# Kernel optimization log

Hardware: AMD Instinct MI355X
Metric: run time of the kernel (lower is better)

## Reference

```python
import jax, jax.numpy as jnp
import numpy as np

B, C, H, W, OC, K = 8, 256, 120, 120, 256, 3


def setup_inputs() -> dict:
    key = jax.random.key(0)
    ks = jax.random.split(key, 6)
    x = jax.random.normal(ks[0], (B, C, H, W), jnp.float32)
    y = jax.random.normal(ks[1], (B, C, H, W), jnp.float32)
    # generate_kernel: 1x1 conv in_yC -> in_xC (weight stored as (out, in))
    gen_w = jax.random.normal(ks[2], (C, C), jnp.float32) * (1.0 / np.sqrt(C))
    gen_b = jax.random.normal(ks[3], (C,), jnp.float32) * 0.01
    # fuse: 3x3 conv in_xC -> out_C, padding 1
    fuse_w = jax.random.normal(ks[4], (OC, C, 3, 3), jnp.float32) * (1.0 / np.sqrt(C * 9))
    fuse_b = jax.random.normal(ks[5], (OC,), jnp.float32) * 0.01
    return {"x": x, "y": y, "gen_w": gen_w, "gen_b": gen_b,
            "fuse_w": fuse_w, "fuse_b": fuse_b}


def reference(x, y, gen_w, gen_b, fuse_w, fuse_b):
    b, c, h, w = x.shape
    # AdaptiveAvgPool2d(K): H,W divisible by K -> uniform average pooling
    yp = y.reshape(b, c, K, h // K, K, w // K).mean(axis=(3, 5))  # (B,C,K,K)
    # 1x1 conv to generate per-sample per-channel kernels
    kernel = jnp.einsum('oc,bcij->boij', gen_w, yp) + gen_b[None, :, None, None]
    # dynamic depthwise conv: groups = B*C, padding 1 (cross-correlation, as torch)
    xg = x.reshape(1, b * c, h, w)
    kg = kernel.reshape(b * c, 1, K, K)
    dn = jax.lax.conv_dimension_numbers(xg.shape, kg.shape, ('NCHW', 'OIHW', 'NCHW'))
    out = jax.lax.conv_general_dilated(
        xg, kg, window_strides=(1, 1), padding=((1, 1), (1, 1)),
        dimension_numbers=dn, feature_group_count=b * c)
    out = out.reshape(b, c, h, w)
    # fuse: dense 3x3 conv C -> OC, padding 1, with bias
    dn2 = jax.lax.conv_dimension_numbers(out.shape, fuse_w.shape, ('NCHW', 'OIHW', 'NCHW'))
    res = jax.lax.conv_general_dilated(
        out, fuse_w, window_strides=(1, 1), padding=((1, 1), (1, 1)),
        dimension_numbers=dn2)
    return res + fuse_b[None, :, None, None]
```

## Files before the change

### kernel.cpp

```cpp
#include <hip/hip_runtime.h>
#include <hip/hip_bf16.h>
#include <stdint.h>

#define TB 8
#define TC 256
#define TH 120
#define TW 120
#define THW 14400
#define TOC 256
#define PH 122
#define PW 122

typedef short bf16x8 __attribute__((ext_vector_type(8)));
typedef float f32x4 __attribute__((ext_vector_type(4)));

#define OUTP_BYTES ((size_t)TB * PH * PW * TC * 2)
#define YP_OFF     OUTP_BYTES
#define DK_OFF     (YP_OFF + (size_t)TB * TC * 9 * 4)
#define WP_OFF     (DK_OFF + (size_t)TB * TC * 9 * 4)

__global__ void zero_halo_kernel(char* __restrict__ outP) {
    int i = blockIdx.x * 256 + threadIdx.x;
    int pos_idx = i >> 5, part = i & 31;
    int b = pos_idx / 484; int k = pos_idx - b * 484;
    int h, w;
    if (k < 122)      { h = 0;   w = k; }
    else if (k < 244) { h = 121; w = k - 122; }
    else { int m = k - 244; h = 1 + (m >> 1); w = (m & 1) ? 121 : 0; }
    size_t pos = ((size_t)b * PH + h) * PW + w;
    uint4 z; z.x = 0u; z.y = 0u; z.z = 0u; z.w = 0u;
    *(uint4*)(outP + pos * 512 + part * 16) = z;
}

__global__ __launch_bounds__(128) void pool_kernel(const float* __restrict__ y,
                                                   float* __restrict__ yp) {
    int bc = blockIdx.x, t = threadIdx.x;
    __shared__ float pr[120][4];
    __shared__ float p2[9][8];
    const float* src = y + (size_t)bc * THW;
    if (t < 120) {
        const float4* row = (const float4*)(src + t * TW);
        float s0 = 0.f, s1 = 0.f, s2 = 0.f;
        #pragma unroll
        for (int j = 0; j < 10; ++j)  { float4 v = row[j]; s0 += (v.x + v.y) + (v.z + v.w); }
        #pragma unroll
        for (int j = 10; j < 20; ++j) { float4 v = row[j]; s1 += (v.x + v.y) + (v.z + v.w); }
        #pragma unroll
        for (int j = 20; j < 30; ++j) { float4 v = row[j]; s2 += (v.x + v.y) + (v.z + v.w); }
        pr[t][0] = s0; pr[t][1] = s1; pr[t][2] = s2;
    }
    __syncthreads();
    if (t < 72) {
        int bin = t >> 3, ch = t & 7;
        int bh = bin / 3, bw = bin - bh * 3;
        float a = 0.f;
        #pragma unroll
        for (int r = 0; r < 5; ++r) a += pr[bh * 40 + ch * 5 + r][bw];
        p2[bin][ch] = a;
    }
    __syncthreads();
    if (t < 9) {
        float a = 0.f;
        #pragma unroll
        for (int j = 0; j < 8; ++j) a += p2[t][j];
        yp[bc * 9 + t] = a * (1.f / 1600.f);
    }
}

__global__ __launch_bounds__(256) void gen_kernel(const float* __restrict__ yp,
        const float* __restrict__ gen_w, const float* __restrict__ gen_b,
        float* __restrict__ dk) {
    int blk = blockIdx.x;
    int b = blk >> 3, ocg = blk & 7;
    int t = threadIdx.x;
    int ocl = t & 31, cseg = t >> 5;
    int oc = ocg * 32 + ocl;
    __shared__ float yps[TC * 9];
    for (int i = t; i < TC * 9; i += 256) yps[i] = yp[b * TC * 9 + i];
    __syncthreads();
    float acc[9];
    #pragma unroll
    for (int j = 0; j < 9; ++j) acc[j] = 0.f;
    const float* wrow = gen_w + (size_t)oc * TC + cseg * 32;
    for (int c = 0; c < 32; ++c) {
        float w = wrow[c];
        const float* yrow = &yps[(cseg * 32 + c) * 9];
        #pragma unroll
        for (int j = 0; j < 9; ++j) acc[j] += w * yrow[j];
    }
    __shared__ float red[8][32][9];
    #pragma unroll
    for (int j = 0; j < 9; ++j) red[cseg][ocl][j] = acc[j];
    __syncthreads();
    for (int st = 4; st > 0; st >>= 1) {
        if (cseg < st) {
            #pragma unroll
            for (int j = 0; j < 9; ++j) red[cseg][ocl][j] += red[cseg + st][ocl][j];
        }
        __syncthreads();
    }
    if (cseg == 0) {
        float bias = gen_b[oc];
        #pragma unroll
        for (int j = 0; j < 9; ++j)
            dk[((size_t)b * TC + oc) * 9 + j] = red[0][ocl][j] + bias;
    }
}

__global__ __launch_bounds__(1024) void dw_kernel(const float* __restrict__ x,
        const float* __restrict__ dk, __hip_bfloat16* __restrict__ outP) {
    int bid = blockIdx.x;
    int hs = bid & 7;
    int cc = (bid >> 3) & 7;
    int b  = bid >> 6;
    int t = threadIdx.x;
    int c  = t >> 5;
    int wq = t & 31;
    bool active = wq < 30;
    int w0 = wq * 4;
    int cg = cc * 32 + c;
    const float* xp = x + (size_t)(b * TC + cg) * THW;
    const float* dkp = dk + (size_t)(b * TC + cg) * 9;
    float k0[3], k1[3], k2[3];
    #pragma unroll
    for (int j = 0; j < 3; ++j) { k0[j] = dkp[j]; k1[j] = dkp[3 + j]; k2[j] = dkp[6 + j]; }

    __shared__ __align__(16) __hip_bfloat16 stage[2][2][32][124];

    int h0 = hs * 15;
    float A[6], B[6], C[6];
    auto loadrow = [&](int hh, float* V) {
        if (hh < 0 || hh >= TH) {
            #pragma unroll
            for (int j = 0; j < 6; ++j) V[j] = 0.f;
            return;
        }
        const float* row = xp + hh * TW;
        float4 v = *(const float4*)(row + w0);
        V[1] = v.x; V[2] = v.y; V[3] = v.z; V[4] = v.w;
        V[0] = (wq > 0)  ? row[w0 - 1] : 0.f;
        V[5] = (wq < 29) ? row[w0 + 4] : 0.f;
    };
    auto comp = [&](int r, int par, int sub) {
        if (!active) return;
        loadrow(h0 + r + 1, C);
        ushort4 pk;
        #pragma unroll
        for (int i = 0; i < 4; ++i) {
            float o = A[i] * k0[0] + A[i + 1] * k0[1] + A[i + 2] * k0[2]
                    + B[i] * k1[0] + B[i + 1] * k1[1] + B[i + 2] * k1[2]
                    + C[i] * k2[0] + C[i + 1] * k2[1] + C[i + 2] * k2[2];
            __hip_bfloat16 hb = __float2bfloat16(o);
            ushort u = *(ushort*)&hb;
            if (i == 0) pk.x = u; else if (i == 1) pk.y = u;
            else if (i == 2) pk.z = u; else pk.w = u;
        }
        *(ushort4*)&stage[par][sub][c][w0] = pk;
        #pragma unroll
        for (int j = 0; j < 6; ++j) { A[j] = B[j]; B[j] = C[j]; }
    };
    auto flushrow = [&](int r, int par, int sub, int tt) {
        int w = tt >> 2, part = tt & 3;
        ushort vals[8];
        #pragma unroll
        for (int j = 0; j < 8; ++j) vals[j] = *(const ushort*)&stage[par][sub][part * 8 + j][w];
        uint4 o;
        o.x = (uint)vals[0] | ((uint)vals[1] << 16);
        o.y = (uint)vals[2] | ((uint)vals[3] << 16);
        o.z = (uint)vals[4] | ((uint)vals[5] << 16);
        o.w = (uint)vals[6] | ((uint)vals[7] << 16);
        size_t pos = ((size_t)b * PH + (h0 + r + 1)) * PW + (w + 1);
        *(uint4*)((char*)outP + pos * 512 + cc * 64 + part * 16) = o;
    };

    if (active) { loadrow(h0 - 1, A); loadrow(h0, B); }
    comp(0, 0, 0); comp(1, 0, 1);
    __syncthreads();
    #pragma unroll 1
    for (int p = 1; p < 8; ++p) {
        int r0 = 2 * p;
        comp(r0, p & 1, 0);
        if (r0 + 1 < 15) comp(r0 + 1, p & 1, 1);
        if (t < 960) {
            int fr = t >= 480 ? 1 : 0;
            int tt = t - fr * 480;
            flushrow(2 * (p - 1) + fr, (p - 1) & 1, fr, tt);
        }
        __syncthreads();
    }
    if (t < 480) flushrow(14, 1, 0, t);
}

__global__ void wprep_kernel(const float* __restrict__ fuse_w, __hip_bfloat16* __restrict__ Wp) {
    int i = blockIdx.x * 256 + threadIdx.x;
    int ij = i >> 16;
    int oc = (i >> 8) & 255;
    int c  = i & 255;
    Wp[i] = __float2bfloat16(fuse_w[(oc * 256 + c) * 9 + ij]);
}

typedef const __attribute__((address_space(1))) char* gas_t;
typedef __attribute__((address_space(3))) char* las_t;
__device__ __forceinline__ void gload16(const char* g, char* l) {
    __builtin_amdgcn_global_load_lds((gas_t)g, (las_t)l, 16, 0, 0);
}

__global__ __launch_bounds__(256, 2) void gemm_kernel(
        const __hip_bfloat16* __restrict__ outP,
        const __hip_bfloat16* __restrict__ Wp,
        const float* __restrict__ fuse_b,
        float* __restrict__ res) {
    __shared__ __align__(16) char lds[2][32768];
    const int t = threadIdx.x;
    const int lane = t & 63;
    const int wv = t >> 6;
    const int wo = wv >> 1;
    const int wm = wv & 1;

    const int bid0 = blockIdx.x;
    const int logical = (bid0 & 7) * 225 + (bid0 >> 3);
    const int bn = logical & 1;
    const int bm = logical >> 1;

    const char* gI = (const char*)outP;
    const char* gW = (const char*)Wp;

    const int rbp = (((lane & 7) ^ (lane >> 3)) << 4);
    int srcI[4], srcW[4];
    #pragma unroll
    for (int q = 0; q < 4; ++q) {
        int p = (q * 4 + wv) * 8 + (lane >> 3);
        int m = bm * 128 + p;
        int b = m / THW; int r = m - b * THW;
        int h = r / TW;  int w = r - h * TW;
        srcI[q] = (((b * PH + h) * PW + w) << 9) + rbp;
        srcW[q] = ((bn * 128 + p) << 9) + rbp;
    }
    const int segBase = wv * 1024;

    int aWb[4], aWs[4], aIb[4], aIs[4];
    #pragma unroll
    for (int i = 0; i < 4; ++i) {
        int rw = wo * 64 + i * 16 + (lane & 15);
        aWb[i] = rw * 128; aWs[i] = (rw & 7) << 4;
        int ri = wm * 64 + i * 16 + (lane & 15);
        aIb[i] = ri * 128; aIs[i] = (ri & 7) << 4;
    }
    const int klo = (lane >> 4) << 4;

    f32x4 acc[4][4];
    #pragma unroll
    for (int i = 0; i < 4; ++i) {
        #pragma unroll
        for (int j = 0; j < 4; ++j) {
            f32x4 z = {0.f, 0.f, 0.f, 0.f};
            acc[i][j] = z;
        }
    }

    auto step_offs = [&](int s, int& offI, int& offW) {
        int ij = s >> 2;
        int c0b = (s & 3) << 7;
        int di = ij / 3, dj = ij - (ij / 3) * 3;
        offI = ((di * PW + dj) << 9) + c0b;
        offW = (ij << 17) + c0b;
    };
    auto STAGE = [&](int buf, int s) {
        int offI, offW; step_offs(s, offI, offW);
        char* LI = &lds[buf][0];
        char* LW = &lds[buf][16384];
        #pragma unroll
        for (int q = 0; q < 4; ++q) {
            gload16(gI + srcI[q] + offI, LI + segBase + q * 4096);
            gload16(gW + srcW[q] + offW, LW + segBase + q * 4096);
        }
    };
    auto COMPUTE = [&](int buf) {
        const char* LI = &lds[buf][0];
        const char* LW = &lds[buf][16384];
        #pragma unroll
        for (int kk = 0; kk < 2; ++kk) {
            int ck = kk * 64 + klo;
            bf16x8 wf[4], iff[4];
            #pragma unroll
            for (int i = 0; i < 4; ++i)
                wf[i] = *(const bf16x8*)(LW + aWb[i] + (ck ^ aWs[i]));
            #pragma unroll
            for (int i = 0; i < 4; ++i)
                iff[i] = *(const bf16x8*)(LI + aIb[i] + (ck ^ aIs[i]));
            __builtin_amdgcn_s_setprio(1);
            #pragma unroll
            for (int o = 0; o < 4; ++o) {
                #pragma unroll
                for (int mi = 0; mi < 4; ++mi)
                    acc[o][mi] = __builtin_amdgcn_mfma_f32_16x16x32_bf16(
                        wf[o], iff[mi], acc[o][mi], 0, 0, 0);
            }
            __builtin_amdgcn_s_setprio(0);
        }
    };

    STAGE(0, 0);
    #pragma unroll 1
    for (int s = 0; s < 35; ++s) {
        int cur = s & 1;
        STAGE(cur ^ 1, s + 1);
        asm volatile("s_waitcnt vmcnt(8)" ::: "memory");
        __builtin_amdgcn_s_barrier();
        asm volatile("" ::: "memory");
        COMPUTE(cur);
        asm volatile("" ::: "memory");
        __builtin_amdgcn_s_barrier();
        asm volatile("" ::: "memory");
    }
    asm volatile("s_waitcnt vmcnt(0)" ::: "memory");
    __builtin_amdgcn_s_barrier();
    asm volatile("" ::: "memory");
    COMPUTE(1);

    int baseM[4];
    #pragma unroll
    for (int mt = 0; mt < 4; ++mt) {
        int m = bm * 128 + wm * 64 + mt * 16 + (lane & 15);
        int b = m / THW; int r = m - b * THW;
        baseM[mt] = b * (TOC * THW) + r;
    }
    const int ocb0 = bn * 128 + wo * 64 + ((lane >> 4) << 2);
    float bias[4][4];
    #pragma unroll
    for (int o = 0; o < 4; ++o) {
        #pragma unroll
        for (int g = 0; g < 4; ++g)
            bias[o][g] = fuse_b[ocb0 + o * 16 + g];
    }
    #pragma unroll
    for (int o = 0; o < 4; ++o) {
        #pragma unroll
        for (int mt = 0; mt < 4; ++mt) {
            #pragma unroll
            for (int g = 0; g < 4; ++g)
                res[baseM[mt] + (ocb0 + o * 16 + g) * THW] = acc[o][mt][g] + bias[o][g];
        }
    }
}

extern "C" void kernel_launch(void* const* d_in, const int* in_sizes, int n_in,
                              void* d_out, int out_size, void* d_ws, size_t ws_size,
                              hipStream_t stream) {
    const float* x      = (const float*)d_in[0];
    const float* y      = (const float*)d_in[1];
    const float* gen_w  = (const float*)d_in[2];
    const float* gen_b  = (const float*)d_in[3];
    const float* fuse_w = (const float*)d_in[4];
    const float* fuse_b = (const float*)d_in[5];
    float* out = (float*)d_out;
    char* ws = (char*)d_ws;

    __hip_bfloat16* outP = (__hip_bfloat16*)(ws);
    float* yp = (float*)(ws + YP_OFF);
    float* dk = (float*)(ws + DK_OFF);
    __hip_bfloat16* Wp = (__hip_bfloat16*)(ws + WP_OFF);

    zero_halo_kernel<<<484, 256, 0, stream>>>((char*)outP);
    pool_kernel<<<TB * TC, 128, 0, stream>>>(y, yp);
    gen_kernel<<<64, 256, 0, stream>>>(yp, gen_w, gen_b, dk);
    wprep_kernel<<<2304, 256, 0, stream>>>(fuse_w, Wp);
    dw_kernel<<<512, 1024, 0, stream>>>(x, dk, outP);
    gemm_kernel<<<1800, 256, 0, stream>>>(outP, Wp, fuse_b, out);
}
```

Before: 223.9 us.

## Merge halo-zero and weight-prep kernels; restructure GEMM to 2 waves single-buffered

Fuses the halo zeroing and weight conversion into one launch, saving a kernel launch. The implicit-GEMM kernel drops from 4 waves with double-buffered LDS to 2 waves per block. Each wave now computes a larger 128x64 tile with 32 accumulators, and the block uses a single 32KB LDS buffer with no overlap between loads and MFMA. The intent is more register-level reuse and more resident blocks per CU, at the cost of serializing global-to-LDS loads against compute.

```diff
diff --git a/kernel.cpp b/kernel.cpp
--- a/kernel.cpp
+++ b/kernel.cpp
@@ -19,17 +19,28 @@
 #define DK_OFF     (YP_OFF + (size_t)TB * TC * 9 * 4)
 #define WP_OFF     (DK_OFF + (size_t)TB * TC * 9 * 4)
 
-__global__ void zero_halo_kernel(char* __restrict__ outP) {
-    int i = blockIdx.x * 256 + threadIdx.x;
-    int pos_idx = i >> 5, part = i & 31;
-    int b = pos_idx / 484; int k = pos_idx - b * 484;
-    int h, w;
-    if (k < 122)      { h = 0;   w = k; }
-    else if (k < 244) { h = 121; w = k - 122; }
-    else { int m = k - 244; h = 1 + (m >> 1); w = (m & 1) ? 121 : 0; }
-    size_t pos = ((size_t)b * PH + h) * PW + w;
-    uint4 z; z.x = 0u; z.y = 0u; z.z = 0u; z.w = 0u;
-    *(uint4*)(outP + pos * 512 + part * 16) = z;
+__global__ void prep_kernel(const float* __restrict__ fuse_w,
+                            __hip_bfloat16* __restrict__ Wp,
+                            char* __restrict__ outP) {
+    int blk = blockIdx.x;
+    if (blk < 484) {
+        int i = blk * 256 + threadIdx.x;
+        int pos_idx = i >> 5, part = i & 31;
+        int b = pos_idx / 484; int k = pos_idx - b * 484;
+        int h, w;
+        if (k < 122)      { h = 0;   w = k; }
+        else if (k < 244) { h = 121; w = k - 122; }
+        else { int m = k - 244; h = 1 + (m >> 1); w = (m & 1) ? 121 : 0; }
+        size_t pos = ((size_t)b * PH + h) * PW + w;
+        uint4 z; z.x = 0u; z.y = 0u; z.z = 0u; z.w = 0u;
+        *(uint4*)(outP + pos * 512 + part * 16) = z;
+    } else {
+        int i = (blk - 484) * 256 + threadIdx.x;
+        int ij = i >> 16;
+        int oc = (i >> 8) & 255;
+        int c  = i & 255;
+        Wp[i] = __float2bfloat16(fuse_w[(oc * 256 + c) * 9 + ij]);
+    }
 }
 
 __global__ __launch_bounds__(128) void pool_kernel(const float* __restrict__ y,
@@ -191,31 +202,26 @@
     if (t < 480) flushrow(14, 1, 0, t);
 }
 
-__global__ void wprep_kernel(const float* __restrict__ fuse_w, __hip_bfloat16* __restrict__ Wp) {
-    int i = blockIdx.x * 256 + threadIdx.x;
-    int ij = i >> 16;
-    int oc = (i >> 8) & 255;
-    int c  = i & 255;
-    Wp[i] = __float2bfloat16(fuse_w[(oc * 256 + c) * 9 + ij]);
-}
-
 typedef const __attribute__((address_space(1))) char* gas_t;
 typedef __attribute__((address_space(3))) char* las_t;
 __device__ __forceinline__ void gload16(const char* g, char* l) {
     __builtin_amdgcn_global_load_lds((gas_t)g, (las_t)l, 16, 0, 0);
 }
-
-__global__ __launch_bounds__(256, 2) void gemm_kernel(
+__device__ __forceinline__ void barrier_() {
+    asm volatile("" ::: "memory");
+    __builtin_amdgcn_s_barrier();
+    asm volatile("" ::: "memory");
+}
+
+__global__ __launch_bounds__(128) void gemm_kernel(
         const __hip_bfloat16* __restrict__ outP,
         const __hip_bfloat16* __restrict__ Wp,
         const float* __restrict__ fuse_b,
         float* __restrict__ res) {
-    __shared__ __align__(16) char lds[2][32768];
+    __shared__ __align__(16) char lds[32768];
     const int t = threadIdx.x;
     const int lane = t & 63;
-    const int wv = t >> 6;
-    const int wo = wv >> 1;
-    const int wm = wv & 1;
+    const int wn = t >> 6;
 
     const int bid0 = blockIdx.x;
     const int logical = (bid0 & 7) * 225 + (bid0 >> 3);
@@ -225,121 +231,101 @@
     const char* gI = (const char*)outP;
     const char* gW = (const char*)Wp;
 
-    const int rbp = (((lane & 7) ^ (lane >> 3)) << 4);
-    int srcI[4], srcW[4];
-    #pragma unroll
-    for (int q = 0; q < 4; ++q) {
-        int p = (q * 4 + wv) * 8 + (lane >> 3);
+    const int srb = (((t & 7) ^ ((t >> 3) & 7)) << 4);
+    int srcA[8], srcB[8];
+    #pragma unroll
+    for (int q = 0; q < 8; ++q) {
+        int p = q * 16 + (t >> 3);
         int m = bm * 128 + p;
         int b = m / THW; int r = m - b * THW;
         int h = r / TW;  int w = r - h * TW;
-        srcI[q] = (((b * PH + h) * PW + w) << 9) + rbp;
-        srcW[q] = ((bn * 128 + p) << 9) + rbp;
-    }
-    const int segBase = wv * 1024;
-
-    int aWb[4], aWs[4], aIb[4], aIs[4];
-    #pragma unroll
-    for (int i = 0; i < 4; ++i) {
-        int rw = wo * 64 + i * 16 + (lane & 15);
-        aWb[i] = rw * 128; aWs[i] = (rw & 7) << 4;
-        int ri = wm * 64 + i * 16 + (lane & 15);
-        aIb[i] = ri * 128; aIs[i] = (ri & 7) << 4;
-    }
+        srcA[q] = (((b * PH + h) * PW + w) << 9) + srb;
+        srcB[q] = ((bn * 128 + p) << 9) + srb;
+    }
+
+    const int sw  = (lane & 7) << 4;
     const int klo = (lane >> 4) << 4;
-
-    f32x4 acc[4][4];
-    #pragma unroll
-    for (int i = 0; i < 4; ++i) {
-        #pragma unroll
-        for (int j = 0; j < 4; ++j) {
-            f32x4 z = {0.f, 0.f, 0.f, 0.f};
-            acc[i][j] = z;
-        }
-    }
-
-    auto step_offs = [&](int s, int& offI, int& offW) {
+    int aA[8], aB[4];
+    #pragma unroll
+    for (int f = 0; f < 8; ++f) aA[f] = (f * 16 + (lane & 15)) * 128;
+    #pragma unroll
+    for (int g = 0; g < 4; ++g) aB[g] = 16384 + (wn * 64 + g * 16 + (lane & 15)) * 128;
+
+    f32x4 acc[8][4];
+    #pragma unroll
+    for (int f = 0; f < 8; ++f) {
+        #pragma unroll
+        for (int g = 0; g < 4; ++g) { f32x4 z = {0.f,0.f,0.f,0.f}; acc[f][g] = z; }
+    }
+
+    auto STAGE = [&](int s) {
         int ij = s >> 2;
         int c0b = (s & 3) << 7;
-        int di = ij / 3, dj = ij - (ij / 3) * 3;
-        offI = ((di * PW + dj) << 9) + c0b;
-        offW = (ij << 17) + c0b;
-    };
-    auto STAGE = [&](int buf, int s) {
-        int offI, offW; step_offs(s, offI, offW);
-        char* LI = &lds[buf][0];
-        char* LW = &lds[buf][16384];
-        #pragma unroll
-        for (int q = 0; q < 4; ++q) {
-            gload16(gI + srcI[q] + offI, LI + segBase + q * 4096);
-            gload16(gW + srcW[q] + offW, LW + segBase + q * 4096);
-        }
-    };
-    auto COMPUTE = [&](int buf) {
-        const char* LI = &lds[buf][0];
-        const char* LW = &lds[buf][16384];
+        int di = ij / 3, dj = ij - di * 3;
+        int offI = ((di * PW + dj) << 9) + c0b;
+        int offW = (ij << 17) + c0b;
+        #pragma unroll
+        for (int q = 0; q < 8; ++q)
+            gload16(gI + srcA[q] + offI, lds + q * 2048 + t * 16);
+        #pragma unroll
+        for (int q = 0; q < 8; ++q)
+            gload16(gW + srcB[q] + offW, lds + 16384 + q * 2048 + t * 16);
+    };
+    auto COMPUTE = [&]() {
         #pragma unroll
         for (int kk = 0; kk < 2; ++kk) {
-            int ck = kk * 64 + klo;
-            bf16x8 wf[4], iff[4];
-            #pragma unroll
-            for (int i = 0; i < 4; ++i)
-                wf[i] = *(const bf16x8*)(LW + aWb[i] + (ck ^ aWs[i]));
-            #pragma unroll
-            for (int i = 0; i < 4; ++i)
-                iff[i] = *(const bf16x8*)(LI + aIb[i] + (ck ^ aIs[i]));
+            int cx = (kk * 64 + klo) ^ sw;
+            bf16x8 fA[8], fB[4];
+            #pragma unroll
+            for (int f = 0; f < 8; ++f) fA[f] = *(const bf16x8*)(lds + aA[f] + cx);
+            #pragma unroll
+            for (int g = 0; g < 4; ++g) fB[g] = *(const bf16x8*)(lds + aB[g] + cx);
             __builtin_amdgcn_s_setprio(1);
             #pragma unroll
-            for (int o = 0; o < 4; ++o) {
+            for (int f = 0; f < 8; ++f) {
                 #pragma unroll
-                for (int mi = 0; mi < 4; ++mi)
-                    acc[o][mi] = __builtin_amdgcn_mfma_f32_16x16x32_bf16(
-                        wf[o], iff[mi], acc[o][mi], 0, 0, 0);
+                for (int g = 0; g < 4; ++g)
+                    acc[f][g] = __builtin_amdgcn_mfma_f32_16x16x32_bf16(
+                        fB[g], fA[f], acc[f][g], 0, 0, 0);
             }
             __builtin_amdgcn_s_setprio(0);
         }
     };
 
-    STAGE(0, 0);
+    STAGE(0);
     #pragma unroll 1
     for (int s = 0; s < 35; ++s) {
-        int cur = s & 1;
-        STAGE(cur ^ 1, s + 1);
-        asm volatile("s_waitcnt vmcnt(8)" ::: "memory");
-        __builtin_amdgcn_s_barrier();
-        asm volatile("" ::: "memory");
-        COMPUTE(cur);
-        asm volatile("" ::: "memory");
-        __builtin_amdgcn_s_barrier();
-        asm volatile("" ::: "memory");
+        asm volatile("s_waitcnt vmcnt(0)" ::: "memory");
+        barrier_();
+        COMPUTE();
+        barrier_();
+        STAGE(s + 1);
     }
     asm volatile("s_waitcnt vmcnt(0)" ::: "memory");
-    __builtin_amdgcn_s_barrier();
-    asm volatile("" ::: "memory");
-    COMPUTE(1);
-
-    int baseM[4];
-    #pragma unroll
-    for (int mt = 0; mt < 4; ++mt) {
-        int m = bm * 128 + wm * 64 + mt * 16 + (lane & 15);
+    barrier_();
+    COMPUTE();
+
+    int baseM[8];
+    #pragma unroll
+    for (int f = 0; f < 8; ++f) {
+        int m = bm * 128 + f * 16 + (lane & 15);
         int b = m / THW; int r = m - b * THW;
-        baseM[mt] = b * (TOC * THW) + r;
-    }
-    const int ocb0 = bn * 128 + wo * 64 + ((lane >> 4) << 2);
+        baseM[f] = b * (TOC * THW) + r;
+    }
+    const int oc0 = bn * 128 + wn * 64 + ((lane >> 4) << 2);
     float bias[4][4];
     #pragma unroll
-    for (int o = 0; o < 4; ++o) {
-        #pragma unroll
-        for (int g = 0; g < 4; ++g)
-            bias[o][g] = fuse_b[ocb0 + o * 16 + g];
-    }
-    #pragma unroll
-    for (int o = 0; o < 4; ++o) {
-        #pragma unroll
-        for (int mt = 0; mt < 4; ++mt) {
-            #pragma unroll
-            for (int g = 0; g < 4; ++g)
-                res[baseM[mt] + (ocb0 + o * 16 + g) * THW] = acc[o][mt][g] + bias[o][g];
+    for (int g = 0; g < 4; ++g) {
+        #pragma unroll
+        for (int j = 0; j < 4; ++j) bias[g][j] = fuse_b[oc0 + g * 16 + j];
+    }
+    #pragma unroll
+    for (int g = 0; g < 4; ++g) {
+        #pragma unroll
+        for (int f = 0; f < 8; ++f) {
+            #pragma unroll
+            for (int j = 0; j < 4; ++j)
+                res[baseM[f] + (oc0 + g * 16 + j) * THW] = acc[f][g][j] + bias[g][j];
         }
     }
 }
@@ -361,10 +347,9 @@
     float* dk = (float*)(ws + DK_OFF);
     __hip_bfloat16* Wp = (__hip_bfloat16*)(ws + WP_OFF);
 
-    zero_halo_kernel<<<484, 256, 0, stream>>>((char*)outP);
+    prep_kernel<<<2788, 256, 0, stream>>>(fuse_w, Wp, (char*)outP);
     pool_kernel<<<TB * TC, 128, 0, stream>>>(y, yp);
     gen_kernel<<<64, 256, 0, stream>>>(yp, gen_w, gen_b, dk);
-    wprep_kernel<<<2304, 256, 0, stream>>>(fuse_w, Wp);
     dw_kernel<<<512, 1024, 0, stream>>>(x, dk, outP);
-    gemm_kernel<<<1800, 256, 0, stream>>>(outP, Wp, fuse_b, out);
-}
+    gemm_kernel<<<1800, 128, 0, stream>>>(outP, Wp, fuse_b, out);
+}
```

Result: slower. 349.6 us (+56.1%).
